# Optimization experiments

Measured on AMD Instinct MI355X. Metric: run time of the kernel, lower is better.

## Reference

```python
import jax, jax.numpy as jnp
import numpy as np
import math

B, T, C, NH, LEVEL = 2, 2048, 1024, 16, 3


def _build_sets(T, level):
    # hierarchical dyadic sets: levels `level`..floor(log2(T)), step 2^l
    sets = []
    levelmax = int(math.floor(math.log2(T)))
    for l in range(level, levelmax + 1):
        step = 2 ** l
        for i in range(T // step):
            sets.append((i * step, (i + 1) * step - 1))
    b = np.asarray(sets, dtype=np.int32)
    return b[:, 0], b[:, 1]


def setup_inputs() -> dict:
    key = jax.random.key(0)
    kx, kw1, kw2 = jax.random.split(key, 3)
    x = jax.random.normal(kx, (B, T, C), dtype=jnp.float32)
    # torch nn.Linear stores weight as (out_features, in_features); y = x @ W.T
    W_attn = jax.random.normal(kw1, (3 * C, C), dtype=jnp.float32) * (C ** -0.5)
    W_proj = jax.random.normal(kw2, (C, C), dtype=jnp.float32) * (C ** -0.5)
    return {"x": x, "W_attn": W_attn, "W_proj": W_proj}


def _get_slice(xc, l_idx, r_idx):
    # xc: (B,NH,T,hs) cumulative sums; returns sum over [l_idx, r_idx]
    r = xc[:, :, r_idx, :]
    l = xc[:, :, l_idx - 1, :] * (l_idx >= 1)[None, None, :, None].astype(xc.dtype)
    return r - l


def _forward(x, W_attn, W_proj):
    hs = C // NH
    scale = hs ** -0.5
    qkv = x @ W_attn.T                      # (B,T,3C)
    q, k, v = jnp.split(qkv, 3, axis=2)
    heads = lambda t: t.reshape(B, T, NH, hs).transpose(0, 2, 1, 3)  # (B,NH,T,hs)
    q, k, v = heads(q), heads(k), heads(v)
    phi = lambda t: jax.nn.elu(t) + 1.0     # feature_map = 'elu_plus'
    q_phi, k_phi = phi(q), phi(k)
    k_cum = jnp.cumsum(k_phi, axis=2)
    v_cum = jnp.cumsum(v, axis=2)

    l_np, r_np = _build_sets(T, LEVEL)
    l_idx, r_idx = jnp.asarray(l_np), jnp.asarray(r_np)
    K = _get_slice(k_cum, l_idx, r_idx)     # (B,NH,S,hs)
    V = _get_slice(v_cum, l_idx, r_idx)

    t_idx = jnp.arange(T)
    mask = t_idx[:, None] >= r_idx[None, :]                 # (T,S)
    logits = jnp.einsum('bhtd,bhsd->bhts', q, K) * scale    # raw q here (as in source)
    logits = jnp.where(mask[None, None], logits, -jnp.inf)

    # tail term over last (t mod 2^level)+1 tokens, uses q_phi
    Lmin = 2 ** LEVEL
    tail_len = t_idx % Lmin + 1
    l_tail = t_idx - tail_len + 1
    K_tail = _get_slice(k_cum, l_tail, t_idx)               # (B,NH,T,hs)
    V_tail = _get_slice(v_cum, l_tail, t_idx)
    tail_logit = jnp.sum(q_phi * K_tail, axis=-1) * scale   # (B,NH,T)

    full = jnp.concatenate([logits, tail_logit[..., None]], axis=-1)
    att = jax.nn.softmax(full, axis=-1)
    out = jnp.einsum('bhts,bhsd->bhtd', att[..., :-1], V) + att[..., -1:] * V_tail
    out = out.transpose(0, 2, 1, 3).reshape(B, T, C)
    return out @ W_proj.T


def reference(x, W_attn, W_proj):
    return _forward(x, W_attn, W_proj)
```

## Files before the change

### kernel.cpp

```cpp
#include <hip/hip_runtime.h>
#include <hip/hip_bf16.h>
#include <stdint.h>

#define B_    2
#define T_    2048
#define CD    1024
#define NH_   16
#define HS_   64
#define NSETS 511
#define NSP   512
#define QKV_LD 3072
#define NEGBIG (-3.4e38f)

typedef __attribute__((ext_vector_type(8))) short  short8;
typedef __attribute__((ext_vector_type(4))) float  f32x4;

__device__ __forceinline__ unsigned short f2bf(float f) {
  unsigned u = __float_as_uint(f);
  unsigned r = 0x7FFFu + ((u >> 16) & 1u);
  return (unsigned short)((u + r) >> 16);
}
__device__ __forceinline__ float bf2f(unsigned short h) {
  return __uint_as_float(((unsigned)h) << 16);
}
__device__ __forceinline__ float elu1(float x) {
  return x > 0.f ? x + 1.f : __expf(x);
}
__device__ __forceinline__ void gload16(const unsigned short* g, short* l) {
  __builtin_amdgcn_global_load_lds(
      (const __attribute__((address_space(1))) unsigned int*)g,
      (__attribute__((address_space(3))) unsigned int*)l, 16, 0, 0);
}

__global__ __launch_bounds__(256) void split3_kernel(
    const float* __restrict__ x, const float* __restrict__ Wa,
    const float* __restrict__ Wp,
    unsigned short* __restrict__ xh, unsigned short* __restrict__ xl,
    unsigned short* __restrict__ wah, unsigned short* __restrict__ wal,
    unsigned short* __restrict__ wph) {
  int bid = blockIdx.x;
  const float* src; unsigned short *hi, *lo; int base;
  if (bid < 16384)      { src = x;  hi = xh;  lo = xl;  base = bid; }
  else if (bid < 24576) { src = Wa; hi = wah; lo = wal; base = bid - 16384; }
  else if (bid < 28672) { src = Wa; hi = wah; lo = nullptr; base = bid - 16384; }
  else                  { src = Wp; hi = wph; lo = nullptr; base = bid - 28672; }
  int i = base * 256 + threadIdx.x;
  float v = src[i];
  unsigned short h = f2bf(v);
  hi[i] = h;
  if (lo) lo[i] = f2bf(v - bf2f(h));
}

template<int SPLIT>
__device__ __forceinline__ void gemm_body(
    short* lds,
    const unsigned short* __restrict__ Ah, const unsigned short* __restrict__ Al,
    const unsigned short* __restrict__ Bh, const unsigned short* __restrict__ Bl,
    float* __restrict__ Cmat, int K, int ldc, int row0, int col0)
{
  const int tid  = threadIdx.x;
  const int lane = tid & 63;
  const int w    = tid >> 6;
  const int wr   = w >> 1, wc = w & 1;

  f32x4 acc[4][4];
  #pragma unroll
  for (int a = 0; a < 4; ++a)
    #pragma unroll
    for (int b = 0; b < 4; ++b)
      acc[a][b] = (f32x4){0.f, 0.f, 0.f, 0.f};

  const int rlane = lane & 15;
  const int kgrp  = lane >> 4;
  const int rsw   = (kgrp ^ (rlane & 3) ^ ((rlane >> 2) & 3)) << 4;

  const int slr = lane >> 2;
  const int sch = (lane & 3) ^ (slr & 3) ^ ((slr >> 2) & 3);

  const unsigned short* ssrc;
  size_t srb;
  short* sbase;
  if (SPLIT) {
    ssrc = (w == 0) ? Ah : (w == 1) ? Bh : (w == 2) ? Al : Bl;
    srb  = (w & 1) ? (size_t)col0 : (size_t)row0;
    sbase = &lds[w * 4096];
  } else {
    ssrc = (w & 1) ? Bh : Ah;
    srb  = (w & 1) ? (size_t)col0 : (size_t)row0;
    sbase = &lds[(w & 1) * 4096 + (w >> 1) * 2048];
    srb += (size_t)(w >> 1) * 64;
  }

  for (int kt = 0; kt < K; kt += 32) {
    __syncthreads();
    const unsigned short* g0 = ssrc + (srb + slr) * K + kt + (sch << 3);
    if (SPLIT) {
      #pragma unroll
      for (int i = 0; i < 8; ++i)
        gload16(g0 + (size_t)i * 16 * K, sbase + i * 512);
    } else {
      #pragma unroll
      for (int i = 0; i < 4; ++i)
        gload16(g0 + (size_t)i * 16 * K, sbase + i * 512);
    }
    __syncthreads();

    short8 aH[4], bH[4], aL[4], bL[4];
    #pragma unroll
    for (int m = 0; m < 4; ++m) {
      int r    = wr * 64 + m * 16 + rlane;
      int cidx = wc * 64 + m * 16 + rlane;
      aH[m] = *(const short8*)((const char*)lds + r * 64 + rsw);
      bH[m] = *(const short8*)((const char*)lds + 8192 + cidx * 64 + rsw);
      if (SPLIT) {
        aL[m] = *(const short8*)((const char*)lds + 16384 + r * 64 + rsw);
        bL[m] = *(const short8*)((const char*)lds + 24576 + cidx * 64 + rsw);
      }
    }
    #pragma unroll
    for (int mm = 0; mm < 4; ++mm)
      #pragma unroll
      for (int nn = 0; nn < 4; ++nn) {
        acc[mm][nn] = __builtin_amdgcn_mfma_f32_16x16x32_bf16(aH[mm], bH[nn], acc[mm][nn], 0, 0, 0);
        if (SPLIT) {
          acc[mm][nn] = __builtin_amdgcn_mfma_f32_16x16x32_bf16(aH[mm], bL[nn], acc[mm][nn], 0, 0, 0);
          acc[mm][nn] = __builtin_amdgcn_mfma_f32_16x16x32_bf16(aL[mm], bH[nn], acc[mm][nn], 0, 0, 0);
        }
      }
  }

  const int rl = (lane >> 4) * 4;
  const int cl = lane & 15;
  #pragma unroll
  for (int mm = 0; mm < 4; ++mm)
    #pragma unroll
    for (int nn = 0; nn < 4; ++nn)
      #pragma unroll
      for (int r = 0; r < 4; ++r) {
        int row = row0 + wr * 64 + mm * 16 + rl + r;
        int col = col0 + wc * 64 + nn * 16 + cl;
        Cmat[(size_t)row * ldc + col] = acc[mm][nn][r];
      }
}

template<int SPLIT>
__global__ __launch_bounds__(256) void gemm_bt(
    const unsigned short* __restrict__ Ah, const unsigned short* __restrict__ Al,
    const unsigned short* __restrict__ Bh, const unsigned short* __restrict__ Bl,
    float* __restrict__ Cmat, int M, int N, int K, int ldc)
{
  constexpr int NT = SPLIT ? 4 : 2;
  __shared__ short lds[NT * 4096];
  const int nwg = gridDim.x;
  const int cpx = nwg >> 3;
  const int bid = blockIdx.x;
  const int swb = (bid & 7) * cpx + (bid >> 3);
  const int nbx = N >> 7;
  const int bx = swb % nbx;
  const int by = swb / nbx;
  gemm_body<SPLIT>(lds, Ah, Al, Bh, Bl, Cmat, K, ldc, by * 128, bx * 128);
}

__global__ __launch_bounds__(256) void cs_part(const float* __restrict__ qkv,
                                               float* __restrict__ part) {
  int blk = blockIdx.x;
  int q   = blk & 1;
  int seg = (blk >> 1) & 63;
  int b   = blk >> 7;
  int c   = threadIdx.x * 4;
  const float* src = qkv + (size_t)(b * T_ + seg * 32) * QKV_LD + CD + q * CD + c;
  float4 s = {0.f, 0.f, 0.f, 0.f};
  #pragma unroll 4
  for (int j = 0; j < 32; ++j) {
    float4 v = *(const float4*)(src + (size_t)j * QKV_LD);
    if (q == 0) {
      s.x += elu1(v.x); s.y += elu1(v.y); s.z += elu1(v.z); s.w += elu1(v.w);
    } else {
      s.x += v.x; s.y += v.y; s.z += v.z; s.w += v.w;
    }
  }
  *(float4*)(part + ((size_t)(b * 64 + seg) * 2048) + q * 1024 + c) = s;
}

__global__ __launch_bounds__(256) void cs_final(const float* __restrict__ qkv,
                                                const float* __restrict__ part,
                                                float* __restrict__ kcum,
                                                float* __restrict__ vcum) {
  int blk = blockIdx.x;
  int q   = blk & 1;
  int seg = (blk >> 1) & 63;
  int b   = blk >> 7;
  int c   = threadIdx.x * 4;
  int h   = c >> 6, d = c & 63;
  float4 s = {0.f, 0.f, 0.f, 0.f};
  const float* pb = part + (size_t)(b * 64) * 2048 + q * 1024 + c;
  #pragma unroll 8
  for (int ss = 0; ss < seg; ++ss) {
    float4 p = *(const float4*)(pb + (size_t)ss * 2048);
    s.x += p.x; s.y += p.y; s.z += p.z; s.w += p.w;
  }
  const float* src = qkv + (size_t)(b * T_ + seg * 32) * QKV_LD + CD + q * CD + c;
  float* dst = (q == 0 ? kcum : vcum) + ((size_t)(b * NH_ + h) * T_ + seg * 32) * HS_ + d;
  #pragma unroll 4
  for (int j = 0; j < 32; ++j) {
    float4 v = *(const float4*)(src + (size_t)j * QKV_LD);
    if (q == 0) {
      s.x += elu1(v.x); s.y += elu1(v.y); s.z += elu1(v.z); s.w += elu1(v.w);
    } else {
      s.x += v.x; s.y += v.y; s.z += v.z; s.w += v.w;
    }
    *(float4*)(dst + (size_t)j * HS_) = s;
  }
}

__global__ __launch_bounds__(256) void build_sets2(
    const float* __restrict__ kcum, const float* __restrict__ vcum,
    unsigned short* __restrict__ Ksh, unsigned short* __restrict__ Ksl,
    unsigned short* __restrict__ Vst, int* __restrict__ r_srt)
{
  __shared__ int   lr[64], lli[64];
  __shared__ float vt[64][65];
  const int bh = blockIdx.x >> 3;
  const int s0 = (blockIdx.x & 7) * 64;
  const int tid = threadIdx.x;

  for (int s = tid; s < NSP; s += 256) {
    int r, li, rank;
    if (s == NSETS) { r = 0x7fffffff; li = 0; rank = NSETS; }
    else {
      int lvl = 3, base = 0;
      while (s >= base + (T_ >> lvl)) { base += T_ >> lvl; ++lvl; }
      int i = s - base;
      int m = (i + 1) << lvl;
      r = m - 1; li = i << lvl;
      rank = lvl - 3;
      #pragma unroll
      for (int j = 3; j <= 11; ++j) rank += (m - 8) >> j;
    }
    if (rank >= s0 && rank < s0 + 64) {
      lr[rank - s0]  = r;
      lli[rank - s0] = li;
      if (bh == 0) r_srt[rank] = r;
    }
  }
  __syncthreads();

  const int sl = tid >> 2;
  const int dq = (tid & 3) * 16;
  const int r  = lr[sl], li = lli[sl];
  const size_t orow = ((size_t)(bh << 9) + s0 + sl) * HS_ + dq;
  short8 kh0, kh1, kl0, kl1;
  if (r == 0x7fffffff) {
    #pragma unroll
    for (int j = 0; j < 8; ++j) { kh0[j]=0; kh1[j]=0; kl0[j]=0; kl1[j]=0; }
    #pragma unroll
    for (int j = 0; j < 16; ++j) vt[sl][dq + j] = 0.f;
  } else {
    const float* kr0 = kcum + ((size_t)bh * T_ + r) * HS_ + dq;
    const float* vr0 = vcum + ((size_t)bh * T_ + r) * HS_ + dq;
    const float* kr1 = kcum + ((size_t)bh * T_ + (li - 1)) * HS_ + dq;
    const float* vr1 = vcum + ((size_t)bh * T_ + (li - 1)) * HS_ + dq;
    #pragma unroll
    for (int g = 0; g < 4; ++g) {
      float4 kv = *(const float4*)(kr0 + g * 4);
      float4 vv = *(const float4*)(vr0 + g * 4);
      if (li > 0) {
        float4 k1 = *(const float4*)(kr1 + g * 4);
        float4 v1 = *(const float4*)(vr1 + g * 4);
        kv.x -= k1.x; kv.y -= k1.y; kv.z -= k1.z; kv.w -= k1.w;
        vv.x -= v1.x; vv.y -= v1.y; vv.z -= v1.z; vv.w -= v1.w;
      }
      float ka[4] = {kv.x, kv.y, kv.z, kv.w};
      float va[4] = {vv.x, vv.y, vv.z, vv.w};
      #pragma unroll
      for (int j = 0; j < 4; ++j) {
        int e = g * 4 + j;
        unsigned short h = f2bf(ka[j]);
        unsigned short l = f2bf(ka[j] - bf2f(h));
        if (e < 8) { kh0[e] = (short)h; kl0[e] = (short)l; }
        else       { kh1[e - 8] = (short)h; kl1[e - 8] = (short)l; }
        vt[sl][dq + e] = va[j];
      }
    }
  }
  *(short8*)(Ksh + orow)     = kh0;
  *(short8*)(Ksh + orow + 8) = kh1;
  *(short8*)(Ksl + orow)     = kl0;
  *(short8*)(Ksl + orow + 8) = kl1;
  __syncthreads();

  const int d  = tid >> 2;
  const int sq = (tid & 3) * 16;
  short8 a, b2;
  #pragma unroll
  for (int j = 0; j < 8; ++j) {
    a[j]  = (short)f2bf(vt[sq + j][d]);
    b2[j] = (short)f2bf(vt[sq + 8 + j][d]);
  }
  unsigned short* dst = Vst + ((size_t)(bh << 6) + d) * NSP + s0 + sq;
  *(short8*)dst = a;
  *(short8*)(dst + 8) = b2;
}

__global__ __launch_bounds__(256) void attn_mfma(
    const float* __restrict__ qkv, const float* __restrict__ kcum,
    const float* __restrict__ vcum,
    const unsigned short* __restrict__ Ksh, const unsigned short* __restrict__ Ksl,
    const unsigned short* __restrict__ Vst, const int* __restrict__ r_srt,
    unsigned short* __restrict__ attnb)
{
  __shared__ short Pl[4 * 1024];
  __shared__ short KV[3 * 4096];
  __shared__ int   rs_lds[NSP];

  const int blk = blockIdx.x;
  const int xcd = blk & 7;
  const int j   = blk >> 3;
  const int bh  = xcd * 4 + (j >> 5);
  const int tch = (j + ((j >> 5) << 3)) & 31;
  const int b = bh >> 4, h = bh & 15;
  const int t0 = tch * 64;
  const int tid = threadIdx.x;
  const int lane = tid & 63;
  const int w = tid >> 6;
  const int col = lane & 15;
  const int kgrp = (lane >> 4) * 8;
  const float scale = 0.125f;

  const int srow = lane >> 3;
  const int scsw = ((lane & 7) ^ srow) * 8;

  auto stage_tile = [&](int s0) {
    #pragma unroll
    for (int L = w * 6; L < w * 6 + 6; ++L) {
      int a = L >> 3, i = L & 7;
      const unsigned short* src;
      if (a == 0)      src = Ksh + ((size_t)(bh << 9) + s0 + i * 8 + srow) * 64 + scsw;
      else if (a == 1) src = Ksl + ((size_t)(bh << 9) + s0 + i * 8 + srow) * 64 + scsw;
      else             src = Vst + ((size_t)(bh << 6) + i * 8 + srow) * NSP + s0 + scsw;
      gload16(src, KV + a * 4096 + i * 512 + lane * 8);
    }
  };

  short8 qh[2], ql[2];
  {
    int qrow = t0 + w * 16 + col;
    const float* qr = qkv + (size_t)(b * T_ + qrow) * QKV_LD + h * HS_;
    #pragma unroll
    for (int ks = 0; ks < 2; ++ks) {
      float4 v0 = *(const float4*)(qr + kgrp + ks * 32);
      float4 v1 = *(const float4*)(qr + kgrp + ks * 32 + 4);
      float vv[8] = {v0.x, v0.y, v0.z, v0.w, v1.x, v1.y, v1.z, v1.w};
      #pragma unroll
      for (int jj = 0; jj < 8; ++jj) {
        unsigned short hi = f2bf(vv[jj]);
        qh[ks][jj] = (short)hi;
        ql[ks][jj] = (short)f2bf(vv[jj] - bf2f(hi));
      }
    }
  }
  for (int s = tid; s < NSP; s += 256) rs_lds[s] = r_srt[s];

  int rows[4];
  #pragma unroll
  for (int r = 0; r < 4; ++r) rows[r] = t0 + w * 16 + (lane >> 4) * 4 + r;

  f32x4 O[4];
  float mrun[4], lsum[4];
  #pragma unroll
  for (int f = 0; f < 4; ++f) {
    O[f] = (f32x4){0.f, 0.f, 0.f, 0.f};
    mrun[f] = NEGBIG; lsum[f] = 0.f;
  }

  int nmax = 0;
  #pragma unroll
  for (int jj = 3; jj <= 11; ++jj) nmax += (t0 + 64) >> jj;
  const int ntiles = (nmax + 63) >> 6;

  for (int tile = 0; tile < ntiles; ++tile) {
    const int s0 = tile * 64;
    stage_tile(s0);
    __syncthreads();

    const char* kc = (const char*)KV;
    f32x4 S[4];
    #pragma unroll
    for (int f = 0; f < 4; ++f) S[f] = (f32x4){0.f, 0.f, 0.f, 0.f};

    #pragma unroll
    for (int ks = 0; ks < 2; ++ks) {
      int chnk = (lane >> 4) + ks * 4;
      #pragma unroll
      for (int f = 0; f < 4; ++f) {
        int so = f * 16 + col;
        int kb = so * 128 + ((chnk ^ (so & 7)) << 4);
        short8 bHv = *(const short8*)(kc + kb);
        short8 bLv = *(const short8*)(kc + 8192 + kb);
        S[f] = __builtin_amdgcn_mfma_f32_16x16x32_bf16(qh[ks], bHv, S[f], 0, 0, 0);
        S[f] = __builtin_amdgcn_mfma_f32_16x16x32_bf16(qh[ks], bLv, S[f], 0, 0, 0);
        S[f] = __builtin_amdgcn_mfma_f32_16x16x32_bf16(ql[ks], bHv, S[f], 0, 0, 0);
      }
    }

    int rsv[4];
    #pragma unroll
    for (int f = 0; f < 4; ++f) rsv[f] = rs_lds[s0 + f * 16 + col];

    float zv[4][4];
    #pragma unroll
    for (int f = 0; f < 4; ++f)
      #pragma unroll
      for (int r = 0; r < 4; ++r)
        zv[f][r] = (rsv[f] > rows[r]) ? NEGBIG : S[f][r] * scale;

    float mx[4];
    #pragma unroll
    for (int r = 0; r < 4; ++r)
      mx[r] = fmaxf(fmaxf(zv[0][r], zv[1][r]), fmaxf(zv[2][r], zv[3][r]));
    int pred = (mx[0] <= mrun[0] + 8.f) & (mx[1] <= mrun[1] + 8.f) &
               (mx[2] <= mrun[2] + 8.f) & (mx[3] <= mrun[3] + 8.f);
    if (!__all(pred)) {
      #pragma unroll
      for (int r = 0; r < 4; ++r) {
        float mt = mx[r];
        mt = fmaxf(mt, __shfl_xor(mt, 1));
        mt = fmaxf(mt, __shfl_xor(mt, 2));
        mt = fmaxf(mt, __shfl_xor(mt, 4));
        mt = fmaxf(mt, __shfl_xor(mt, 8));
        float mv = fmaxf(mrun[r], mt);
        float fs = __expf(mrun[r] - mv);
        lsum[r] *= fs;
        #pragma unroll
        for (int f = 0; f < 4; ++f) O[f][r] *= fs;
        mrun[r] = mv;
      }
    }

    char* pw = (char*)Pl + w * 2048;
    #pragma unroll
    for (int r = 0; r < 4; ++r) {
      int rowr = (lane >> 4) * 4 + r;
      int rswz = (rowr & 7) << 4;
      #pragma unroll
      for (int f = 0; f < 4; ++f) {
        float p = __expf(zv[f][r] - mrun[r]);
        p = (rsv[f] > rows[r]) ? 0.f : p;
        lsum[r] += p;
        int addr = (rowr * 128 + (f * 16 + col) * 2) ^ rswz;
        *(unsigned short*)(pw + addr) = f2bf(p);
      }
    }

    #pragma unroll
    for (int ks = 0; ks < 2; ++ks) {
      int chnk = (lane >> 4) + ks * 4;
      int pbyte = (col * 128 + (kgrp + ks * 32) * 2) ^ ((col & 7) << 4);
      short8 pa = *(const short8*)(pw + pbyte);
      #pragma unroll
      for (int f = 0; f < 4; ++f) {
        int dr = f * 16 + col;
        short8 bv = *(const short8*)(kc + 16384 + dr * 128 + ((chnk ^ (dr & 7)) << 4));
        O[f] = __builtin_amdgcn_mfma_f32_16x16x32_bf16(pa, bv, O[f], 0, 0, 0);
      }
    }

    __syncthreads();
  }

  float lrun[4];
  #pragma unroll
  for (int r = 0; r < 4; ++r) {
    float l = lsum[r];
    l += __shfl_xor(l, 1);
    l += __shfl_xor(l, 2);
    l += __shfl_xor(l, 4);
    l += __shfl_xor(l, 8);
    lrun[r] = l;
  }

  float ztail;
  {
    int trow = lane >> 2;
    int t = t0 + w * 16 + trow;
    int d0 = (lane & 3) * 16;
    const float* qr = qkv + (size_t)(b * T_ + t) * QKV_LD + h * HS_ + d0;
    float qv[16];
    #pragma unroll
    for (int jj = 0; jj < 4; ++jj) {
      float4 v = *(const float4*)(qr + jj * 4);
      qv[jj*4+0] = v.x; qv[jj*4+1] = v.y; qv[jj*4+2] = v.z; qv[jj*4+3] = v.w;
    }
    int lt = t & ~7;
    const float* kc1 = kcum + ((size_t)bh * T_ + t) * HS_ + d0;
    float kt[16];
    if (lt > 0) {
      const float* kc0 = kcum + ((size_t)bh * T_ + (lt - 1)) * HS_ + d0;
      #pragma unroll
      for (int jj = 0; jj < 16; ++jj) kt[jj] = kc1[jj] - kc0[jj];
    } else {
      #pragma unroll
      for (int jj = 0; jj < 16; ++jj) kt[jj] = kc1[jj];
    }
    float z = 0.f;
    #pragma unroll
    for (int jj = 0; jj < 16; ++jj) {
      float qp = qv[jj] > 0.f ? qv[jj] + 1.f : __expf(qv[jj]);
      z += qp * kt[jj];
    }
    z += __shfl_xor(z, 1);
    z += __shfl_xor(z, 2);
    ztail = z * scale;
  }

  #pragma unroll
  for (int r = 0; r < 4; ++r) {
    float zt = __shfl(ztail, ((lane >> 4) * 4 + r) * 4);
    float mv = fmaxf(mrun[r], zt);
    float fs = __expf(mrun[r] - mv);
    float pwgt = __expf(zt - mv);
    lrun[r] = lrun[r] * fs + pwgt;
    int tr = rows[r];
    int ltr = tr & ~7;
    #pragma unroll
    for (int f = 0; f < 4; ++f) {
      int d = f * 16 + col;
      float v1 = vcum[((size_t)bh * T_ + tr) * HS_ + d];
      float vt = (ltr > 0) ? v1 - vcum[((size_t)bh * T_ + (ltr - 1)) * HS_ + d] : v1;
      O[f][r] = O[f][r] * fs + pwgt * vt;
    }
  }

  #pragma unroll
  for (int r = 0; r < 4; ++r) {
    float inv = 1.f / lrun[r];
    unsigned short* orow = attnb + (size_t)(b * T_ + rows[r]) * CD + h * HS_;
    #pragma unroll
    for (int f = 0; f < 4; ++f)
      orow[f * 16 + col] = f2bf(O[f][r] * inv);
  }
}

extern "C" void kernel_launch(void* const* d_in, const int* in_sizes, int n_in,
                              void* d_out, int out_size, void* d_ws, size_t ws_size,
                              hipStream_t stream) {
  const float* x  = (const float*)d_in[0];
  const float* Wa = (const float*)d_in[1];
  const float* Wp = (const float*)d_in[2];
  float* out = (float*)d_out;

  char* ws = (char*)d_ws;
  size_t off = 0;
  auto alloc = [&](size_t bytes) -> char* {
    char* p = ws + off;
    off += (bytes + 255) & ~(size_t)255;
    return p;
  };

  const int M = B_ * T_;
  float* qkv  = (float*)alloc((size_t)M * QKV_LD * 4);
  float* kcum = (float*)alloc((size_t)B_ * NH_ * T_ * HS_ * 4);
  float* vcum = (float*)alloc((size_t)B_ * NH_ * T_ * HS_ * 4);
  float* part = (float*)alloc((size_t)B_ * 64 * 2048 * 4);
  unsigned short* wph = (unsigned short*)alloc((size_t)CD * CD * 2);

  char* regionA = alloc((size_t)16777216);
  unsigned short* xh = (unsigned short*)regionA;
  unsigned short* xl = (unsigned short*)(regionA + (size_t)M * CD * 2);
  const size_t SETS_ELEMS = (size_t)B_ * NH_ * NSP * HS_;
  unsigned short* Ksh = (unsigned short*)regionA;
  unsigned short* Ksl = Ksh + SETS_ELEMS;
  unsigned short* Vst = (unsigned short*)(regionA + 2 * SETS_ELEMS * 2);
  int*            r_srt = (int*)(regionA + 3 * SETS_ELEMS * 2);

  char* regionB = alloc((size_t)12582912);
  unsigned short* wah = (unsigned short*)regionB;
  unsigned short* wal = (unsigned short*)(regionB + (size_t)3 * CD * CD * 2);
  unsigned short* attnb = (unsigned short*)regionB;

  split3_kernel<<<dim3(32768), dim3(256), 0, stream>>>(
      x, Wa, Wp, xh, xl, wah, wal, wph);

  gemm_bt<1><<<dim3((2048 / 128) * (M / 128)), dim3(256), 0, stream>>>(
      xh, xl, wah, wal, qkv, M, 2048, CD, QKV_LD);

  gemm_bt<0><<<dim3((1024 / 128) * (M / 128)), dim3(256), 0, stream>>>(
      xh, (const unsigned short*)nullptr, wah + (size_t)2048 * CD,
      (const unsigned short*)nullptr, qkv + 2048, M, 1024, CD, QKV_LD);

  cs_part<<<dim3(B_ * 64 * 2), dim3(256), 0, stream>>>(qkv, part);
  cs_final<<<dim3(B_ * 64 * 2), dim3(256), 0, stream>>>(qkv, part, kcum, vcum);

  build_sets2<<<dim3(B_ * NH_ * 8), dim3(256), 0, stream>>>(
      kcum, vcum, Ksh, Ksl, Vst, r_srt);

  attn_mfma<<<dim3(1024), dim3(256), 0, stream>>>(
      qkv, kcum, vcum, Ksh, Ksl, Vst, r_srt, attnb);

  gemm_bt<0><<<dim3((CD / 128) * (M / 128)), dim3(256), 0, stream>>>(
      attnb, (const unsigned short*)nullptr, wph, (const unsigned short*)nullptr,
      out, M, CD, CD, CD);
}
```

Measured before the change: 203.9 us.

## Use split-bf16 only for Q projection, fp16 MFMA for K/V, narrower tiles

The QKV projection is rearranged. Only the Q columns keep the three-MFMA split-bf16 (hi/lo) emulation, while K and V now use a single fp16 MFMA pass with fp16 copies of x and W. Before, both Q and K used the split path and only V was plain bf16. The GEMM template gains a BN tile width parameter: the Q and output-projection GEMMs use 64-wide tiles so each launches 512 blocks, and the K/V GEMM uses 128-wide tiles. This cuts MFMA work and LDS traffic for K, but lowers precision on the K projection, which feeds the cumulative sums and the logits.

Measured after the change: 185.9 us. -8.8%, faster.

```diff
diff --git a/kernel.cpp b/kernel.cpp
--- a/kernel.cpp
+++ b/kernel.cpp
@@ -14,6 +14,7 @@
 
 typedef __attribute__((ext_vector_type(8))) short  short8;
 typedef __attribute__((ext_vector_type(4))) float  f32x4;
+typedef _Float16 half8v __attribute__((ext_vector_type(8)));
 
 __device__ __forceinline__ unsigned short f2bf(float f) {
   unsigned u = __float_as_uint(f);
@@ -23,6 +24,10 @@
 __device__ __forceinline__ float bf2f(unsigned short h) {
   return __uint_as_float(((unsigned)h) << 16);
 }
+__device__ __forceinline__ unsigned short f2h(float v) {
+  _Float16 h = (_Float16)v;
+  return __builtin_bit_cast(unsigned short, h);
+}
 __device__ __forceinline__ float elu1(float x) {
   return x > 0.f ? x + 1.f : __expf(x);
 }
@@ -36,38 +41,58 @@
     const float* __restrict__ x, const float* __restrict__ Wa,
     const float* __restrict__ Wp,
     unsigned short* __restrict__ xh, unsigned short* __restrict__ xl,
-    unsigned short* __restrict__ wah, unsigned short* __restrict__ wal,
-    unsigned short* __restrict__ wph) {
+    unsigned short* __restrict__ xf,
+    unsigned short* __restrict__ waqh, unsigned short* __restrict__ waql,
+    unsigned short* __restrict__ wakvf, unsigned short* __restrict__ wph) {
   int bid = blockIdx.x;
-  const float* src; unsigned short *hi, *lo; int base;
-  if (bid < 16384)      { src = x;  hi = xh;  lo = xl;  base = bid; }
-  else if (bid < 24576) { src = Wa; hi = wah; lo = wal; base = bid - 16384; }
-  else if (bid < 28672) { src = Wa; hi = wah; lo = nullptr; base = bid - 16384; }
-  else                  { src = Wp; hi = wph; lo = nullptr; base = bid - 28672; }
-  int i = base * 256 + threadIdx.x;
-  float v = src[i];
-  unsigned short h = f2bf(v);
-  hi[i] = h;
-  if (lo) lo[i] = f2bf(v - bf2f(h));
-}
-
-template<int SPLIT>
+  int t = threadIdx.x;
+  if (bid < 16384) {
+    int i = bid * 256 + t;
+    float v = x[i];
+    unsigned short h = f2bf(v);
+    xh[i] = h;
+    xl[i] = f2bf(v - bf2f(h));
+    xf[i] = f2h(v);
+  } else if (bid < 20480) {
+    int i = (bid - 16384) * 256 + t;
+    float v = Wa[i];
+    unsigned short h = f2bf(v);
+    waqh[i] = h;
+    waql[i] = f2bf(v - bf2f(h));
+  } else if (bid < 28672) {
+    int i = (bid - 20480) * 256 + t;
+    wakvf[i] = f2h(Wa[1048576 + i]);
+  } else {
+    int i = (bid - 28672) * 256 + t;
+    wph[i] = f2bf(Wp[i]);
+  }
+}
+
+template<int SPLIT, int BN, int F16>
 __device__ __forceinline__ void gemm_body(
     short* lds,
     const unsigned short* __restrict__ Ah, const unsigned short* __restrict__ Al,
     const unsigned short* __restrict__ Bh, const unsigned short* __restrict__ Bl,
     float* __restrict__ Cmat, int K, int ldc, int row0, int col0)
 {
+  constexpr int NB   = BN / 16;
+  constexpr int ALD  = 8 * (1 + SPLIT);
+  constexpr int TL   = ALD + NB * (1 + SPLIT);
+  constexpr int PW   = TL / 4;
+  constexpr int ASH  = (1 + SPLIT) * 4096;
+  constexpr int ABYT = ASH * 2;
+  constexpr int NC   = BN / 32;
+
   const int tid  = threadIdx.x;
   const int lane = tid & 63;
   const int w    = tid >> 6;
   const int wr   = w >> 1, wc = w & 1;
 
-  f32x4 acc[4][4];
+  f32x4 acc[4][NC];
   #pragma unroll
   for (int a = 0; a < 4; ++a)
     #pragma unroll
-    for (int b = 0; b < 4; ++b)
+    for (int b = 0; b < NC; ++b)
       acc[a][b] = (f32x4){0.f, 0.f, 0.f, 0.f};
 
   const int rlane = lane & 15;
@@ -77,54 +102,50 @@
   const int slr = lane >> 2;
   const int sch = (lane & 3) ^ (slr & 3) ^ ((slr >> 2) & 3);
 
-  const unsigned short* ssrc;
-  size_t srb;
-  short* sbase;
-  if (SPLIT) {
-    ssrc = (w == 0) ? Ah : (w == 1) ? Bh : (w == 2) ? Al : Bl;
-    srb  = (w & 1) ? (size_t)col0 : (size_t)row0;
-    sbase = &lds[w * 4096];
-  } else {
-    ssrc = (w & 1) ? Bh : Ah;
-    srb  = (w & 1) ? (size_t)col0 : (size_t)row0;
-    sbase = &lds[(w & 1) * 4096 + (w >> 1) * 2048];
-    srb += (size_t)(w >> 1) * 64;
-  }
-
   for (int kt = 0; kt < K; kt += 32) {
     __syncthreads();
-    const unsigned short* g0 = ssrc + (srb + slr) * K + kt + (sch << 3);
-    if (SPLIT) {
-      #pragma unroll
-      for (int i = 0; i < 8; ++i)
-        gload16(g0 + (size_t)i * 16 * K, sbase + i * 512);
-    } else {
-      #pragma unroll
-      for (int i = 0; i < 4; ++i)
-        gload16(g0 + (size_t)i * 16 * K, sbase + i * 512);
+    #pragma unroll
+    for (int li = 0; li < PW; ++li) {
+      int L = w * PW + li;
+      const unsigned short* src; int dsts; size_t rowb;
+      if (L < 8)                { src = Ah; rowb = (size_t)row0 + L * 16;       dsts = L * 512; }
+      else if (SPLIT && L < 16) { src = Al; rowb = (size_t)row0 + (L - 8) * 16; dsts = 4096 + (L - 8) * 512; }
+      else {
+        int Lb = L - ALD;
+        if (!SPLIT || Lb < NB) { src = Bh; rowb = (size_t)col0 + Lb * 16;        dsts = ASH + Lb * 512; }
+        else                   { src = Bl; rowb = (size_t)col0 + (Lb - NB) * 16; dsts = ASH + BN * 32 + (Lb - NB) * 512; }
+      }
+      gload16(src + (rowb + slr) * K + kt + (sch << 3), lds + dsts + lane * 8);
     }
     __syncthreads();
 
-    short8 aH[4], bH[4], aL[4], bL[4];
+    short8 aH[4], bH[NC], aL[4], bL[NC];
     #pragma unroll
     for (int m = 0; m < 4; ++m) {
-      int r    = wr * 64 + m * 16 + rlane;
-      int cidx = wc * 64 + m * 16 + rlane;
+      int r = wr * 64 + m * 16 + rlane;
       aH[m] = *(const short8*)((const char*)lds + r * 64 + rsw);
-      bH[m] = *(const short8*)((const char*)lds + 8192 + cidx * 64 + rsw);
-      if (SPLIT) {
-        aL[m] = *(const short8*)((const char*)lds + 16384 + r * 64 + rsw);
-        bL[m] = *(const short8*)((const char*)lds + 24576 + cidx * 64 + rsw);
-      }
+      if (SPLIT) aL[m] = *(const short8*)((const char*)lds + 8192 + r * 64 + rsw);
+    }
+    #pragma unroll
+    for (int n = 0; n < NC; ++n) {
+      int c = wc * (BN / 2) + n * 16 + rlane;
+      bH[n] = *(const short8*)((const char*)lds + ABYT + c * 64 + rsw);
+      if (SPLIT) bL[n] = *(const short8*)((const char*)lds + ABYT + BN * 64 + c * 64 + rsw);
     }
     #pragma unroll
     for (int mm = 0; mm < 4; ++mm)
       #pragma unroll
-      for (int nn = 0; nn < 4; ++nn) {
-        acc[mm][nn] = __builtin_amdgcn_mfma_f32_16x16x32_bf16(aH[mm], bH[nn], acc[mm][nn], 0, 0, 0);
-        if (SPLIT) {
-          acc[mm][nn] = __builtin_amdgcn_mfma_f32_16x16x32_bf16(aH[mm], bL[nn], acc[mm][nn], 0, 0, 0);
-          acc[mm][nn] = __builtin_amdgcn_mfma_f32_16x16x32_bf16(aL[mm], bH[nn], acc[mm][nn], 0, 0, 0);
+      for (int nn = 0; nn < NC; ++nn) {
+        if (F16) {
+          acc[mm][nn] = __builtin_amdgcn_mfma_f32_16x16x32_f16(
+              __builtin_bit_cast(half8v, aH[mm]), __builtin_bit_cast(half8v, bH[nn]),
+              acc[mm][nn], 0, 0, 0);
+        } else {
+          acc[mm][nn] = __builtin_amdgcn_mfma_f32_16x16x32_bf16(aH[mm], bH[nn], acc[mm][nn], 0, 0, 0);
+          if (SPLIT) {
+            acc[mm][nn] = __builtin_amdgcn_mfma_f32_16x16x32_bf16(aH[mm], bL[nn], acc[mm][nn], 0, 0, 0);
+            acc[mm][nn] = __builtin_amdgcn_mfma_f32_16x16x32_bf16(aL[mm], bH[nn], acc[mm][nn], 0, 0, 0);
+          }
         }
       }
   }
@@ -134,31 +155,30 @@
   #pragma unroll
   for (int mm = 0; mm < 4; ++mm)
     #pragma unroll
-    for (int nn = 0; nn < 4; ++nn)
+    for (int nn = 0; nn < NC; ++nn)
       #pragma unroll
       for (int r = 0; r < 4; ++r) {
         int row = row0 + wr * 64 + mm * 16 + rl + r;
-        int col = col0 + wc * 64 + nn * 16 + cl;
+        int col = col0 + wc * (BN / 2) + nn * 16 + cl;
         Cmat[(size_t)row * ldc + col] = acc[mm][nn][r];
       }
 }
 
-template<int SPLIT>
+template<int SPLIT, int BN, int F16>
 __global__ __launch_bounds__(256) void gemm_bt(
     const unsigned short* __restrict__ Ah, const unsigned short* __restrict__ Al,
     const unsigned short* __restrict__ Bh, const unsigned short* __restrict__ Bl,
     float* __restrict__ Cmat, int M, int N, int K, int ldc)
 {
-  constexpr int NT = SPLIT ? 4 : 2;
-  __shared__ short lds[NT * 4096];
+  __shared__ short lds[(1 + SPLIT) * 4096 + (1 + SPLIT) * BN * 32];
   const int nwg = gridDim.x;
   const int cpx = nwg >> 3;
   const int bid = blockIdx.x;
   const int swb = (bid & 7) * cpx + (bid >> 3);
-  const int nbx = N >> 7;
+  const int nbx = N / BN;
   const int bx = swb % nbx;
   const int by = swb / nbx;
-  gemm_body<SPLIT>(lds, Ah, Al, Bh, Bl, Cmat, K, ldc, by * 128, bx * 128);
+  gemm_body<SPLIT, BN, F16>(lds, Ah, Al, Bh, Bl, Cmat, K, ldc, by * 128, bx * BN);
 }
 
 __global__ __launch_bounds__(256) void cs_part(const float* __restrict__ qkv,
@@ -564,6 +584,9 @@
   float* part = (float*)alloc((size_t)B_ * 64 * 2048 * 4);
   unsigned short* wph = (unsigned short*)alloc((size_t)CD * CD * 2);
 
+  unsigned short* xf    = (unsigned short*)kcum;
+  unsigned short* wakvf = (unsigned short*)vcum;
+
   char* regionA = alloc((size_t)16777216);
   unsigned short* xh = (unsigned short*)regionA;
   unsigned short* xl = (unsigned short*)(regionA + (size_t)M * CD * 2);
@@ -574,19 +597,19 @@
   int*            r_srt = (int*)(regionA + 3 * SETS_ELEMS * 2);
 
   char* regionB = alloc((size_t)12582912);
-  unsigned short* wah = (unsigned short*)regionB;
-  unsigned short* wal = (unsigned short*)(regionB + (size_t)3 * CD * CD * 2);
+  unsigned short* waqh = (unsigned short*)regionB;
+  unsigned short* waql = (unsigned short*)(regionB + (size_t)CD * CD * 2);
   unsigned short* attnb = (unsigned short*)regionB;
 
   split3_kernel<<<dim3(32768), dim3(256), 0, stream>>>(
-      x, Wa, Wp, xh, xl, wah, wal, wph);
-
-  gemm_bt<1><<<dim3((2048 / 128) * (M / 128)), dim3(256), 0, stream>>>(
-      xh, xl, wah, wal, qkv, M, 2048, CD, QKV_LD);
-
-  gemm_bt<0><<<dim3((1024 / 128) * (M / 128)), dim3(256), 0, stream>>>(
-      xh, (const unsigned short*)nullptr, wah + (size_t)2048 * CD,
-      (const unsigned short*)nullptr, qkv + 2048, M, 1024, CD, QKV_LD);
+      x, Wa, Wp, xh, xl, xf, waqh, waql, wakvf, wph);
+
+  gemm_bt<1, 64, 0><<<dim3(512), dim3(256), 0, stream>>>(
+      xh, xl, waqh, waql, qkv, M, 1024, CD, QKV_LD);
+
+  gemm_bt<0, 128, 1><<<dim3(512), dim3(256), 0, stream>>>(
+      xf, (const unsigned short*)nullptr, wakvf, (const unsigned short*)nullptr,
+      qkv + 1024, M, 2048, CD, QKV_LD);
 
   cs_part<<<dim3(B_ * 64 * 2), dim3(256), 0, stream>>>(qkv, part);
   cs_final<<<dim3(B_ * 64 * 2), dim3(256), 0, stream>>>(qkv, part, kcum, vcum);
@@ -597,7 +620,7 @@
   attn_mfma<<<dim3(1024), dim3(256), 0, stream>>>(
       qkv, kcum, vcum, Ksh, Ksl, Vst, r_srt, attnb);
 
-  gemm_bt<0><<<dim3((CD / 128) * (M / 128)), dim3(256), 0, stream>>>(
+  gemm_bt<0, 64, 0><<<dim3(512), dim3(256), 0, stream>>>(
       attnb, (const unsigned short*)nullptr, wph, (const unsigned short*)nullptr,
-      out, M, CD, CD, CD);
-}
+      out, M, 1024, CD, CD);
+}
```
